# Kernel optimization log

Measured on AMD Instinct MI355X. Metric: run time of the kernel, lower is better.

## Reference

```python
import jax, jax.numpy as jnp
import numpy as np

B, N1, N2 = 16, 4096, 1024
C1, C2 = 128, 256
IN_CH, OUT_CH = 4096, 256  # fc1 acts on N1 dim due to transpose; BN channels = C2 = OUT_CH
BN_EPS = 1e-5


def setup_inputs() -> dict:
    key = jax.random.key(0)
    ks = jax.random.split(key, 8)
    x1 = jax.random.normal(ks[0], (B, N1, C1), dtype=jnp.float32)
    x2 = jax.random.normal(ks[1], (B, N2, C2), dtype=jnp.float32)
    xyz1 = jax.random.normal(ks[2], (B, N1, 3), dtype=jnp.float32)
    xyz2 = jax.random.normal(ks[3], (B, N2, 3), dtype=jnp.float32)
    # Linear(in_channels=N1 -> out_channels) params, PyTorch default init scale
    bound = 1.0 / np.sqrt(IN_CH)
    W1 = jax.random.uniform(ks[4], (OUT_CH, IN_CH), jnp.float32, -bound, bound)
    b1 = jax.random.uniform(ks[5], (OUT_CH,), jnp.float32, -bound, bound)
    gamma = jnp.ones((OUT_CH,), jnp.float32)
    beta = jnp.zeros((OUT_CH,), jnp.float32)
    return {"x1": x1, "x2": x2, "xyz1": xyz1, "xyz2": xyz2,
            "W1": W1, "b1": b1, "gamma": gamma, "beta": beta}


def _square_distance(src, dst):
    # src: [B,N,3], dst: [B,M,3] -> [B,N,M]
    d = -2.0 * jnp.einsum('bnc,bmc->bnm', src, dst)
    d = d + jnp.sum(src * src, -1)[:, :, None]
    d = d + jnp.sum(dst * dst, -1)[:, None, :]
    return d


def reference(x1, x2, xyz1, xyz2, W1, b1, gamma, beta):
    dists = _square_distance(xyz1, xyz2)              # [B,N1,N2]
    neg3, idx = jax.lax.top_k(-dists, 3)              # 3 smallest distances
    d3 = -neg3                                        # [B,N1,3], ascending
    dist_recip = 1.0 / (d3 + 1e-8)
    weight = dist_recip / jnp.sum(dist_recip, axis=2, keepdims=True)
    gathered = jax.vmap(lambda pts, i: pts[i])(x2, idx)   # [B,N1,3,C2]
    interp = jnp.sum(gathered * weight[..., None], axis=2)  # [B,N1,C2]
    t = jnp.swapaxes(interp, 1, 2)                    # [B,C2,N1]
    y = jnp.einsum('bcn,on->bco', t, W1) + b1         # [B,C2,OUT_CH]
    # BatchNorm1d over channel dim 1 (size C2 == OUT_CH), training-mode batch stats
    mean = jnp.mean(y, axis=(0, 2), keepdims=True)
    var = jnp.mean((y - mean) ** 2, axis=(0, 2), keepdims=True)
    y = (y - mean) / jnp.sqrt(var + BN_EPS)
    y = gamma[None, :, None] * y + beta[None, :, None]
    y = jax.nn.relu(y)
    return jnp.swapaxes(y, 1, 2)                      # [B,OUT_CH,C2]
```

## Files before the change

kernel.cpp:

```cpp
#include <hip/hip_runtime.h>
#include <hip/hip_bf16.h>
#include <float.h>

#define B_    16
#define N1_   4096
#define N2_   1024
#define C2_   256
#define OUT_  256
#define K_    4096
#define SPLITK 8
#define KCH_  (K_ / SPLITK)
#define ZSLAB 1048576

typedef short short8 __attribute__((ext_vector_type(8)));
typedef float float4v __attribute__((ext_vector_type(4)));

static __device__ __forceinline__ unsigned short f32_to_bf16_bits(float v) {
    __hip_bfloat16 h = __float2bfloat16(v);
    return *(unsigned short*)&h;
}

#define TPAD 65
struct KnnSh {
    float4 pts[16][65];
    float  pf[64][49];
};
union ShUnion {
    KnnSh a;
    unsigned short tile[C2_][TPAD];
};

__global__ __launch_bounds__(256) void knn_interp_kernel(
    const float* __restrict__ xyz1,
    const float* __restrict__ xyz2,
    const float* __restrict__ x2,
    unsigned short* __restrict__ interp_t,
    const float* __restrict__ W1,
    unsigned short* __restrict__ W1b,
    float* __restrict__ accum)
{
    __shared__ ShUnion sh;
    __shared__ float rw[64][3];
    __shared__ int   ri[64][3];

    const int bid = blockIdx.x;
    const int t   = threadIdx.x;

    if (bid < 1024) {
        if (bid == 0) {
            accum[t] = 0.0f;
            accum[256 + t] = 0.0f;
        }
        const int i = (bid * 256 + t) * 4;
        float4 v = *(const float4*)(W1 + i);
        ushort4 o;
        o.x = f32_to_bf16_bits(v.x);
        o.y = f32_to_bf16_bits(v.y);
        o.z = f32_to_bf16_bits(v.z);
        o.w = f32_to_bf16_bits(v.w);
        *(ushort4*)(W1b + i) = o;
        return;
    }

    const int rem = bid - 1024;
    const int b   = rem >> 6;
    const int n0  = (rem & 63) * 64;
    const int w   = t >> 6;
    const int l   = t & 63;

    for (int r = 0; r < 4; ++r) {
        int j = r * 256 + t;
        const float* p = xyz2 + ((size_t)b * N2_ + j) * 3;
        float x = p[0], y = p[1], z = p[2];
        sh.a.pts[j >> 6][j & 63] = make_float4(x, y, z, 0.5f * ((x * x + y * y) + z * z));
    }
    __syncthreads();

    const int qg    = l & 15;
    const int slice = (w << 2) | (l >> 4);
    const int jbase = slice << 6;

    const float* qb = xyz1 + ((size_t)b * N1_ + n0 + qg * 4) * 3;
    float4 v0 = ((const float4*)qb)[0];
    float4 v1 = ((const float4*)qb)[1];
    float4 v2 = ((const float4*)qb)[2];
    float qx[4] = {v0.x, v0.w, v1.z, v2.y};
    float qy[4] = {v0.y, v1.x, v1.w, v2.z};
    float qz[4] = {v0.z, v1.y, v2.x, v2.w};

    float ns0[4], ns1[4], ns2[4], ss[4], f[4][3];
    #pragma unroll
    for (int i = 0; i < 4; ++i) {
        ns0[i] = -qx[i]; ns1[i] = -qy[i]; ns2[i] = -qz[i];
        ss[i]  = (qx[i] * qx[i] + qy[i] * qy[i]) + qz[i] * qz[i];
        f[i][0] = FLT_MAX; f[i][1] = FLT_MAX; f[i][2] = FLT_MAX;
    }

    #pragma unroll 2
    for (int jj = 0; jj < 64; ++jj) {
        float4 pq = sh.a.pts[slice][jj];
        int j = jbase + jj;
        #pragma unroll
        for (int i = 0; i < 4; ++i) {
            float acc = fmaf(ns0[i], pq.x, pq.w);
            acc = fmaf(ns1[i], pq.y, acc);
            acc = fmaf(ns2[i], pq.z, acc);
            float dk = fmaxf(fmaf(2.0f, acc, ss[i]), 0.0f);
            float fp = __int_as_float((__float_as_int(dk) & 0xFFFFFC00) | j);
            float nf0 = fminf(fp, f[i][0]);
            float nf1 = __builtin_amdgcn_fmed3f(fp, f[i][0], f[i][1]);
            float nf2 = fminf(f[i][2], fmaxf(fp, f[i][1]));
            f[i][0] = nf0; f[i][1] = nf1; f[i][2] = nf2;
        }
    }

    #pragma unroll
    for (int i = 0; i < 4; ++i)
    #pragma unroll
    for (int r = 0; r < 3; ++r)
        sh.a.pf[qg * 4 + i][slice * 3 + r] = f[i][r];
    __syncthreads();

    if (w == 0) {
        float g0 = FLT_MAX, g1 = FLT_MAX, g2 = FLT_MAX;
        #pragma unroll 4
        for (int s = 0; s < 16; ++s)
        #pragma unroll
        for (int r = 0; r < 3; ++r) {
            float fp = sh.a.pf[l][s * 3 + r];
            float n0v = fminf(fp, g0);
            float n1v = __builtin_amdgcn_fmed3f(fp, g0, g1);
            float n2v = fminf(g2, fmaxf(fp, g1));
            g0 = n0v; g1 = n1v; g2 = n2v;
        }
        int j0 = __float_as_int(g0) & 1023;
        int j1 = __float_as_int(g1) & 1023;
        int j2 = __float_as_int(g2) & 1023;
        const float4 p0 = sh.a.pts[j0 >> 6][j0 & 63];
        const float4 p1 = sh.a.pts[j1 >> 6][j1 & 63];
        const float4 p2 = sh.a.pts[j2 >> 6][j2 & 63];
        float d0 = ss[0] * 0.0f;
        const float s0q = qx[0], s1q = qy[0], s2q = qz[0];
        (void)d0; (void)s0q; (void)s1q; (void)s2q;
        const float* q = xyz1 + ((size_t)b * N1_ + n0 + l) * 3;
        const float s0 = q[0], s1 = q[1], s2 = q[2];
        const float ssl = (s0 * s0 + s1 * s1) + s2 * s2;
        float dd0 = ssl + 2.0f * (p0.w - ((s0 * p0.x + s1 * p0.y) + s2 * p0.z));
        float dd1 = ssl + 2.0f * (p1.w - ((s0 * p1.x + s1 * p1.y) + s2 * p1.z));
        float dd2 = ssl + 2.0f * (p2.w - ((s0 * p2.x + s1 * p2.y) + s2 * p2.z));
        float r0 = 1.0f / (dd0 + 1e-8f);
        float r1 = 1.0f / (dd1 + 1e-8f);
        float r2 = 1.0f / (dd2 + 1e-8f);
        float sden = (r0 + r1) + r2;
        rw[l][0] = r0 / sden;  rw[l][1] = r1 / sden;  rw[l][2] = r2 / sden;
        ri[l][0] = j0;         ri[l][1] = j1;         ri[l][2] = j2;
    }
    __syncthreads();

    for (int p = 0; p < 16; ++p) {
        int nl = p * 4 + w;
        float w0 = rw[nl][0], w1 = rw[nl][1], w2 = rw[nl][2];
        int i0g = ri[nl][0], i1g = ri[nl][1], i2g = ri[nl][2];
        const float4 va = ((const float4*)(x2 + ((size_t)b * N2_ + i0g) * C2_))[l];
        const float4 vb = ((const float4*)(x2 + ((size_t)b * N2_ + i1g) * C2_))[l];
        const float4 vc = ((const float4*)(x2 + ((size_t)b * N2_ + i2g) * C2_))[l];
        float fa[4] = {va.x, va.y, va.z, va.w};
        float fb[4] = {vb.x, vb.y, vb.z, vb.w};
        float fc[4] = {vc.x, vc.y, vc.z, vc.w};
        #pragma unroll
        for (int i = 0; i < 4; ++i) {
            float v = w0 * fa[i];
            v = fmaf(w1, fb[i], v);
            v = fmaf(w2, fc[i], v);
            sh.tile[l * 4 + i][nl] = f32_to_bf16_bits(v);
        }
    }
    __syncthreads();

    for (int r = 0; r < 64; ++r) {
        int c = r * 4 + w;
        interp_t[((size_t)b * C2_ + c) * K_ + n0 + l] = sh.tile[c][l];
    }
}

#define LDA 72
__global__ __launch_bounds__(256) void gemm_kernel(
    const unsigned short* __restrict__ W1b,
    const unsigned short* __restrict__ interp_t,
    float* __restrict__ Zp)
{
    __shared__ unsigned short Alds[128][LDA];
    __shared__ unsigned short Blds[64][LDA];
    const int z  = blockIdx.z;
    const int b  = z >> 3;
    const int kc = z & 7;
    const int o0 = blockIdx.y * 128;
    const int c0 = blockIdx.x * 64;
    const int t = threadIdx.x;
    const int w = t >> 6, l = t & 63;
    const int arow = t >> 1, ahalf = t & 1;
    const int brow = t >> 2, bq = t & 3;
    const int ob = (w >> 1) * 64, cb = (w & 1) * 32;
    const int m = l & 15, kq = l >> 4;

    const unsigned short* Wp = W1b + (size_t)(o0 + arow) * K_ + kc * KCH_ + ahalf * 32;
    const unsigned short* Bp = interp_t + ((size_t)b * C2_ + (c0 + brow)) * K_ + kc * KCH_ + bq * 16;

    float4v acc[4][2] = {};

    uint4 a0 = *(const uint4*)(Wp);
    uint4 a1 = *(const uint4*)(Wp + 8);
    uint4 a2 = *(const uint4*)(Wp + 16);
    uint4 a3 = *(const uint4*)(Wp + 24);
    uint4 b0 = *(const uint4*)(Bp);
    uint4 b1 = *(const uint4*)(Bp + 8);

    for (int kk = 0; kk < KCH_; kk += 64) {
        *(uint4*)&Alds[arow][ahalf * 32]      = a0;
        *(uint4*)&Alds[arow][ahalf * 32 + 8]  = a1;
        *(uint4*)&Alds[arow][ahalf * 32 + 16] = a2;
        *(uint4*)&Alds[arow][ahalf * 32 + 24] = a3;
        *(uint4*)&Blds[brow][bq * 16]         = b0;
        *(uint4*)&Blds[brow][bq * 16 + 8]     = b1;
        __syncthreads();

        if (kk + 64 < KCH_) {
            a0 = *(const uint4*)(Wp + kk + 64);
            a1 = *(const uint4*)(Wp + kk + 72);
            a2 = *(const uint4*)(Wp + kk + 80);
            a3 = *(const uint4*)(Wp + kk + 88);
            b0 = *(const uint4*)(Bp + kk + 64);
            b1 = *(const uint4*)(Bp + kk + 72);
        }

        #pragma unroll
        for (int ks = 0; ks < 64; ks += 32) {
            short8 bf0 = *(const short8*)&Blds[cb + m][ks + kq * 8];
            short8 bf1 = *(const short8*)&Blds[cb + 16 + m][ks + kq * 8];
            #pragma unroll
            for (int mi = 0; mi < 4; ++mi) {
                short8 af = *(const short8*)&Alds[ob + mi * 16 + m][ks + kq * 8];
                acc[mi][0] = __builtin_amdgcn_mfma_f32_16x16x32_bf16(af, bf0, acc[mi][0], 0, 0, 0);
                acc[mi][1] = __builtin_amdgcn_mfma_f32_16x16x32_bf16(af, bf1, acc[mi][1], 0, 0, 0);
            }
        }
        __syncthreads();
    }

    float* Zslab = Zp + (size_t)kc * ZSLAB;
    #pragma unroll
    for (int mi = 0; mi < 4; ++mi)
    #pragma unroll
    for (int ni = 0; ni < 2; ++ni)
    #pragma unroll
    for (int r = 0; r < 4; ++r) {
        int o = o0 + ob + mi * 16 + kq * 4 + r;
        int c = c0 + cb + ni * 16 + m;
        Zslab[((size_t)b * OUT_ + o) * C2_ + c] = acc[mi][ni][r];
    }
}

__global__ __launch_bounds__(256) void reduce_stats_kernel(
    float* __restrict__ Zp, const float* __restrict__ b1,
    float* __restrict__ accum)
{
    const int b  = blockIdx.x >> 4;
    const int oq = blockIdx.x & 15;
    const int c  = threadIdx.x;
    float s = 0.0f, s2 = 0.0f;
    for (int o16 = 0; o16 < 16; ++o16) {
        int o = oq * 16 + o16;
        size_t base = ((size_t)b * OUT_ + o) * C2_ + c;
        float v = b1[o];
        #pragma unroll
        for (int sl = 0; sl < SPLITK; ++sl)
            v += Zp[base + (size_t)sl * ZSLAB];
        Zp[base] = v;
        s += v; s2 += v * v;
    }
    atomicAdd(&accum[c], s);
    atomicAdd(&accum[C2_ + c], s2);
}

__global__ __launch_bounds__(256) void bn_kernel(
    const float* __restrict__ Z, const float* __restrict__ accum,
    const float* __restrict__ gamma, const float* __restrict__ beta,
    float* __restrict__ out)
{
    const int i = (blockIdx.x * 256 + threadIdx.x) * 4;
    float4 z = *(const float4*)(Z + i);
    float vals[4] = {z.x, z.y, z.z, z.w};
    const int cb = i & 255;
    float res[4];
    #pragma unroll
    for (int j = 0; j < 4; ++j) {
        int c = cb + j;
        float mean = accum[c] * (1.0f / 4096.0f);
        float var  = accum[C2_ + c] * (1.0f / 4096.0f) - mean * mean;
        float rstd = 1.0f / sqrtf(var + 1e-5f);
        float v = gamma[c] * ((vals[j] - mean) * rstd) + beta[c];
        res[j] = fmaxf(v, 0.0f);
    }
    *(float4*)(out + i) = make_float4(res[0], res[1], res[2], res[3]);
}

extern "C" void kernel_launch(void* const* d_in, const int* in_sizes, int n_in,
                              void* d_out, int out_size, void* d_ws, size_t ws_size,
                              hipStream_t stream) {
    const float* x2    = (const float*)d_in[1];
    const float* xyz1  = (const float*)d_in[2];
    const float* xyz2  = (const float*)d_in[3];
    const float* W1    = (const float*)d_in[4];
    const float* b1    = (const float*)d_in[5];
    const float* gamma = (const float*)d_in[6];
    const float* beta  = (const float*)d_in[7];

    char* ws = (char*)d_ws;
    unsigned short* interp_t = (unsigned short*)(ws);
    unsigned short* W1b      = (unsigned short*)(ws + 33554432);
    float*          Zp       = (float*)(ws + 35651584);
    float*          accum    = (float*)(ws + 69206016);

    knn_interp_kernel <<<2048, 256, 0, stream>>>(xyz1, xyz2, x2, interp_t,
                                                 W1, W1b, accum);
    gemm_kernel       <<<dim3(4, 2, 128), 256, 0, stream>>>(W1b, interp_t, Zp);
    reduce_stats_kernel<<<256, 256, 0, stream>>>(Zp, b1, accum);
    bn_kernel         <<<1024, 256, 0, stream>>>(Zp, accum, gamma, beta,
                                                 (float*)d_out);
}
```

Before: 158.9 us.

## Merge KNN partial top-3 via wave shuffles and halve transpose tile LDS

Partial top-3 candidates from the 16 lanes sharing a query are now merged in registers with xor-shuffles across lane groups, rather than all being written to LDS for wave 0 to merge. Wave 0 then merges only 4 candidates per query instead of 16. The bf16 transpose tile is split into two 32-column halves, which shrinks the shared-memory union and may raise occupancy. The cost is extra shuffle ALU work and one more barrier round in the transpose/store phase, and global stores now write narrower 32-element row segments.

```diff
diff --git a/kernel.cpp b/kernel.cpp
--- a/kernel.cpp
+++ b/kernel.cpp
@@ -20,14 +20,14 @@
     return *(unsigned short*)&h;
 }
 
-#define TPAD 65
+#define TPAD2 33
 struct KnnSh {
     float4 pts[16][65];
-    float  pf[64][49];
+    float  pf[4][64][3];
 };
 union ShUnion {
     KnnSh a;
-    unsigned short tile[C2_][TPAD];
+    unsigned short tile[C2_][TPAD2];
 };
 
 __global__ __launch_bounds__(256) void knn_interp_kernel(
@@ -115,19 +115,43 @@
     }
 
     #pragma unroll
-    for (int i = 0; i < 4; ++i)
-    #pragma unroll
-    for (int r = 0; r < 3; ++r)
-        sh.a.pf[qg * 4 + i][slice * 3 + r] = f[i][r];
+    for (int x = 16; x <= 32; x <<= 1) {
+        #pragma unroll
+        for (int i = 0; i < 4; ++i) {
+            float h0 = __shfl_xor(f[i][0], x);
+            float h1 = __shfl_xor(f[i][1], x);
+            float h2 = __shfl_xor(f[i][2], x);
+            float t0, t1, t2;
+            t0 = fminf(h0, f[i][0]);
+            t1 = __builtin_amdgcn_fmed3f(h0, f[i][0], f[i][1]);
+            t2 = fminf(f[i][2], fmaxf(h0, f[i][1]));
+            f[i][0] = t0; f[i][1] = t1; f[i][2] = t2;
+            t0 = fminf(h1, f[i][0]);
+            t1 = __builtin_amdgcn_fmed3f(h1, f[i][0], f[i][1]);
+            t2 = fminf(f[i][2], fmaxf(h1, f[i][1]));
+            f[i][0] = t0; f[i][1] = t1; f[i][2] = t2;
+            t0 = fminf(h2, f[i][0]);
+            t1 = __builtin_amdgcn_fmed3f(h2, f[i][0], f[i][1]);
+            t2 = fminf(f[i][2], fmaxf(h2, f[i][1]));
+            f[i][0] = t0; f[i][1] = t1; f[i][2] = t2;
+        }
+    }
+    if ((l >> 4) == 0) {
+        #pragma unroll
+        for (int i = 0; i < 4; ++i)
+        #pragma unroll
+        for (int r = 0; r < 3; ++r)
+            sh.a.pf[w][l * 4 + i][r] = f[i][r];
+    }
     __syncthreads();
 
     if (w == 0) {
         float g0 = FLT_MAX, g1 = FLT_MAX, g2 = FLT_MAX;
-        #pragma unroll 4
-        for (int s = 0; s < 16; ++s)
+        #pragma unroll
+        for (int p = 0; p < 4; ++p)
         #pragma unroll
         for (int r = 0; r < 3; ++r) {
-            float fp = sh.a.pf[l][s * 3 + r];
+            float fp = sh.a.pf[p][l][r];
             float n0v = fminf(fp, g0);
             float n1v = __builtin_amdgcn_fmed3f(fp, g0, g1);
             float n2v = fminf(g2, fmaxf(fp, g1));
@@ -139,9 +163,6 @@
         const float4 p0 = sh.a.pts[j0 >> 6][j0 & 63];
         const float4 p1 = sh.a.pts[j1 >> 6][j1 & 63];
         const float4 p2 = sh.a.pts[j2 >> 6][j2 & 63];
-        float d0 = ss[0] * 0.0f;
-        const float s0q = qx[0], s1q = qy[0], s2q = qz[0];
-        (void)d0; (void)s0q; (void)s1q; (void)s2q;
         const float* q = xyz1 + ((size_t)b * N1_ + n0 + l) * 3;
         const float s0 = q[0], s1 = q[1], s2 = q[2];
         const float ssl = (s0 * s0 + s1 * s1) + s2 * s2;
@@ -157,29 +178,34 @@
     }
     __syncthreads();
 
-    for (int p = 0; p < 16; ++p) {
-        int nl = p * 4 + w;
-        float w0 = rw[nl][0], w1 = rw[nl][1], w2 = rw[nl][2];
-        int i0g = ri[nl][0], i1g = ri[nl][1], i2g = ri[nl][2];
-        const float4 va = ((const float4*)(x2 + ((size_t)b * N2_ + i0g) * C2_))[l];
-        const float4 vb = ((const float4*)(x2 + ((size_t)b * N2_ + i1g) * C2_))[l];
-        const float4 vc = ((const float4*)(x2 + ((size_t)b * N2_ + i2g) * C2_))[l];
-        float fa[4] = {va.x, va.y, va.z, va.w};
-        float fb[4] = {vb.x, vb.y, vb.z, vb.w};
-        float fc[4] = {vc.x, vc.y, vc.z, vc.w};
-        #pragma unroll
-        for (int i = 0; i < 4; ++i) {
-            float v = w0 * fa[i];
-            v = fmaf(w1, fb[i], v);
-            v = fmaf(w2, fc[i], v);
-            sh.tile[l * 4 + i][nl] = f32_to_bf16_bits(v);
-        }
-    }
-    __syncthreads();
-
-    for (int r = 0; r < 64; ++r) {
-        int c = r * 4 + w;
-        interp_t[((size_t)b * C2_ + c) * K_ + n0 + l] = sh.tile[c][l];
+    for (int half = 0; half < 2; ++half) {
+        for (int p = 0; p < 8; ++p) {
+            int nlc = p * 4 + w;
+            int nl  = half * 32 + nlc;
+            float w0 = rw[nl][0], w1 = rw[nl][1], w2 = rw[nl][2];
+            int i0g = ri[nl][0], i1g = ri[nl][1], i2g = ri[nl][2];
+            const float4 va = ((const float4*)(x2 + ((size_t)b * N2_ + i0g) * C2_))[l];
+            const float4 vb = ((const float4*)(x2 + ((size_t)b * N2_ + i1g) * C2_))[l];
+            const float4 vc = ((const float4*)(x2 + ((size_t)b * N2_ + i2g) * C2_))[l];
+            float fa[4] = {va.x, va.y, va.z, va.w};
+            float fb[4] = {vb.x, vb.y, vb.z, vb.w};
+            float fc[4] = {vc.x, vc.y, vc.z, vc.w};
+            #pragma unroll
+            for (int i = 0; i < 4; ++i) {
+                float v = w0 * fa[i];
+                v = fmaf(w1, fb[i], v);
+                v = fmaf(w2, fc[i], v);
+                sh.tile[l * 4 + i][nlc] = f32_to_bf16_bits(v);
+            }
+        }
+        __syncthreads();
+
+        for (int r = 0; r < 32; ++r) {
+            int c   = r * 8 + w * 2 + (l >> 5);
+            int col = l & 31;
+            interp_t[((size_t)b * C2_ + c) * K_ + n0 + half * 32 + col] = sh.tile[c][col];
+        }
+        __syncthreads();
     }
 }
 
```

Result: slower. 169.6 us (+6.7%).

## Load GEMM tiles directly into LDS with swizzled layout

Applied to the files above, without the earlier changes.

Replaces the register-staged global-to-LDS copy in the split-K GEMM with direct global_load_lds transfers into an unpadded, XOR-swizzled shared tile, and adjusts the MFMA fragment reads to match the swizzle. This removes the VGPR staging and the padded layout, cutting register pressure and LDS write instructions. It also drops the register prefetch of the next tile, so global loads are no longer overlapped with the MFMA work of the previous step. Some dead code in the KNN kernel is removed.

```diff
diff --git a/kernel.cpp b/kernel.cpp
--- a/kernel.cpp
+++ b/kernel.cpp
@@ -18,6 +18,12 @@
 static __device__ __forceinline__ unsigned short f32_to_bf16_bits(float v) {
     __hip_bfloat16 h = __float2bfloat16(v);
     return *(unsigned short*)&h;
+}
+
+static __device__ __forceinline__ void gload16(const void* g, void* l) {
+    __builtin_amdgcn_global_load_lds(
+        (const __attribute__((address_space(1))) unsigned int*)g,
+        (__attribute__((address_space(3))) unsigned int*)l, 16, 0, 0);
 }
 
 #define TPAD 65
@@ -139,9 +145,6 @@
         const float4 p0 = sh.a.pts[j0 >> 6][j0 & 63];
         const float4 p1 = sh.a.pts[j1 >> 6][j1 & 63];
         const float4 p2 = sh.a.pts[j2 >> 6][j2 & 63];
-        float d0 = ss[0] * 0.0f;
-        const float s0q = qx[0], s1q = qy[0], s2q = qz[0];
-        (void)d0; (void)s0q; (void)s1q; (void)s2q;
         const float* q = xyz1 + ((size_t)b * N1_ + n0 + l) * 3;
         const float s0 = q[0], s1 = q[1], s2 = q[2];
         const float ssl = (s0 * s0 + s1 * s1) + s2 * s2;
@@ -183,14 +186,13 @@
     }
 }
 
-#define LDA 72
 __global__ __launch_bounds__(256) void gemm_kernel(
     const unsigned short* __restrict__ W1b,
     const unsigned short* __restrict__ interp_t,
     float* __restrict__ Zp)
 {
-    __shared__ unsigned short Alds[128][LDA];
-    __shared__ unsigned short Blds[64][LDA];
+    __shared__ unsigned short Alds[128 * 64];
+    __shared__ unsigned short Blds[64 * 64];
     const int z  = blockIdx.z;
     const int b  = z >> 3;
     const int kc = z & 7;
@@ -198,48 +200,39 @@
     const int c0 = blockIdx.x * 64;
     const int t = threadIdx.x;
     const int w = t >> 6, l = t & 63;
-    const int arow = t >> 1, ahalf = t & 1;
-    const int brow = t >> 2, bq = t & 3;
     const int ob = (w >> 1) * 64, cb = (w & 1) * 32;
     const int m = l & 15, kq = l >> 4;
 
-    const unsigned short* Wp = W1b + (size_t)(o0 + arow) * K_ + kc * KCH_ + ahalf * 32;
-    const unsigned short* Bp = interp_t + ((size_t)b * C2_ + (c0 + brow)) * K_ + kc * KCH_ + bq * 16;
+    const int rs  = l >> 3;
+    const int ch  = l & 7;
+    const int sch = ch ^ rs;
+
+    const unsigned short* Abase = W1b + (size_t)o0 * K_ + kc * KCH_ + sch * 8;
+    const unsigned short* Bbase = interp_t + ((size_t)b * C2_ + c0) * K_ + kc * KCH_ + sch * 8;
 
     float4v acc[4][2] = {};
 
-    uint4 a0 = *(const uint4*)(Wp);
-    uint4 a1 = *(const uint4*)(Wp + 8);
-    uint4 a2 = *(const uint4*)(Wp + 16);
-    uint4 a3 = *(const uint4*)(Wp + 24);
-    uint4 b0 = *(const uint4*)(Bp);
-    uint4 b1 = *(const uint4*)(Bp + 8);
-
     for (int kk = 0; kk < KCH_; kk += 64) {
-        *(uint4*)&Alds[arow][ahalf * 32]      = a0;
-        *(uint4*)&Alds[arow][ahalf * 32 + 8]  = a1;
-        *(uint4*)&Alds[arow][ahalf * 32 + 16] = a2;
-        *(uint4*)&Alds[arow][ahalf * 32 + 24] = a3;
-        *(uint4*)&Blds[brow][bq * 16]         = b0;
-        *(uint4*)&Blds[brow][bq * 16 + 8]     = b1;
+        #pragma unroll
+        for (int i = 0; i < 4; ++i) {
+            int s = w + i * 4;
+            gload16(Abase + (size_t)(s * 8 + rs) * K_ + kk, &Alds[s * 512 + l * 8]);
+        }
+        #pragma unroll
+        for (int i = 0; i < 2; ++i) {
+            int s = w + i * 4;
+            gload16(Bbase + (size_t)(s * 8 + rs) * K_ + kk, &Blds[s * 512 + l * 8]);
+        }
         __syncthreads();
 
-        if (kk + 64 < KCH_) {
-            a0 = *(const uint4*)(Wp + kk + 64);
-            a1 = *(const uint4*)(Wp + kk + 72);
-            a2 = *(const uint4*)(Wp + kk + 80);
-            a3 = *(const uint4*)(Wp + kk + 88);
-            b0 = *(const uint4*)(Bp + kk + 64);
-            b1 = *(const uint4*)(Bp + kk + 72);
-        }
-
         #pragma unroll
         for (int ks = 0; ks < 64; ks += 32) {
-            short8 bf0 = *(const short8*)&Blds[cb + m][ks + kq * 8];
-            short8 bf1 = *(const short8*)&Blds[cb + 16 + m][ks + kq * 8];
+            const int swz = ((kq + (ks >> 3)) ^ (m & 7)) << 3;
+            short8 bf0 = *(const short8*)&Blds[(cb + m) * 64 + swz];
+            short8 bf1 = *(const short8*)&Blds[(cb + 16 + m) * 64 + swz];
             #pragma unroll
             for (int mi = 0; mi < 4; ++mi) {
-                short8 af = *(const short8*)&Alds[ob + mi * 16 + m][ks + kq * 8];
+                short8 af = *(const short8*)&Alds[(ob + mi * 16 + m) * 64 + swz];
                 acc[mi][0] = __builtin_amdgcn_mfma_f32_16x16x32_bf16(af, bf0, acc[mi][0], 0, 0, 0);
                 acc[mi][1] = __builtin_amdgcn_mfma_f32_16x16x32_bf16(af, bf1, acc[mi][1], 0, 0, 0);
             }
```

Result: no change. 156.8 us (-1.3%).
